# Performance work log

Hardware: AMD Instinct MI355X
Metric: run time of the kernel (lower is better)

The kernel has to match this reference:

```python
import jax, jax.numpy as jnp
import numpy as np

TOPK, ALPHA, BETA, EPS = 13, 1.0, 6.0, 1e-9


def _iou(gt, pr):
    # gt: [B,n,4] xyxy, pr: [B,L,4] xyxy -> [B,n,L]
    gx1, gy1, gx2, gy2 = [gt[..., i][:, :, None] for i in range(4)]
    px1, py1, px2, py2 = [pr[..., i][:, None, :] for i in range(4)]
    iw = jnp.maximum(jnp.minimum(gx2, px2) - jnp.maximum(gx1, px1), 0.0)
    ih = jnp.maximum(jnp.minimum(gy2, py2) - jnp.maximum(gy1, py1), 0.0)
    inter = iw * ih
    area_g = (gx2 - gx1) * (gy2 - gy1)
    area_p = (px2 - px1) * (py2 - py1)
    return inter / (area_g + area_p - inter + 1e-9)


def _points_in_gts(points, gt):
    # points: [L,2], gt: [B,n,4] -> float mask [B,n,L]
    x = points[:, 0][None, None, :]
    y = points[:, 1][None, None, :]
    x1, y1, x2, y2 = [gt[..., i][:, :, None] for i in range(4)]
    dmin = jnp.minimum(jnp.minimum(x - x1, y - y1), jnp.minimum(x2 - x, y2 - y))
    return (dmin > EPS).astype(gt.dtype)


def _gather_topk_anchors(metrics, pad_gt_mask):
    # metrics: [B,n,L] -> float mask [B,n,L] of top-k anchors per gt
    B, n, L = metrics.shape
    _, topk_idxs = jax.lax.top_k(metrics, TOPK)            # [B,n,TOPK]
    mask = pad_gt_mask.astype(bool)                        # [B,n,1]
    topk_idxs = jnp.where(mask, topk_idxs, 0)
    base = (jnp.arange(B * n) * L).reshape(B, n, 1)
    flat = (topk_idxs + base).reshape(-1)
    counts = jnp.zeros(B * n * L, metrics.dtype).at[flat].add(1.0).reshape(B, n, L)
    # anchors hit more than once (only possible via masked-to-0 dup) are dropped
    return jnp.where(counts > 1, 0.0, counts)


def _assigner(pred_scores, pred_bboxes, anchor_points, gt_labels, gt_bboxes, pad_gt_mask, bg_index):
    B, L, C = pred_scores.shape
    n = gt_bboxes.shape[1]
    lbl = gt_labels[..., 0]                                # [B,n]

    ious = _iou(gt_bboxes, pred_bboxes)                    # [B,n,L]
    # bbox_cls_scores[b,g,l] = pred_scores[b,l,gt_labels[b,g]]
    bbox_cls_scores = jnp.take_along_axis(
        pred_scores.transpose(0, 2, 1),                    # [B,C,L]
        jnp.broadcast_to(lbl[:, :, None], (B, n, L)), axis=1)
    align = (bbox_cls_scores ** ALPHA) * (ious ** BETA)    # [B,n,L]

    is_in_gts = _points_in_gts(anchor_points, gt_bboxes)   # [B,n,L]
    is_in_topk = _gather_topk_anchors(align * is_in_gts, pad_gt_mask)
    mask_pos = is_in_topk * is_in_gts * pad_gt_mask        # [B,n,L]
    mask_pos_sum = mask_pos.sum(axis=-2)                   # [B,L]

    # resolve anchors assigned to multiple gts by max IoU (no-op where sum<=1)
    is_max_iou = (jnp.argmax(ious, axis=1)[:, None, :]
                  == jnp.arange(n)[None, :, None]).astype(ious.dtype)
    mask_pos = jnp.where(mask_pos_sum[:, None, :] > 1, is_max_iou, mask_pos)
    mask_pos_sum = mask_pos.sum(axis=-2)

    agi = jnp.argmax(mask_pos, axis=-2)                    # [B,L]
    assigned_labels = jnp.take_along_axis(lbl, agi, axis=1)
    assigned_labels = jnp.where(mask_pos_sum > 0, assigned_labels,
                                jnp.full_like(assigned_labels, bg_index))
    assigned_bboxes = jnp.take_along_axis(
        gt_bboxes, jnp.broadcast_to(agi[..., None], (B, L, 4)), axis=1)

    oh = jax.nn.one_hot(assigned_labels, C + 1, dtype=pred_scores.dtype)
    keep = jnp.array([i for i in range(C + 1) if i != bg_index])
    assigned_scores = oh[..., keep]                        # [B,L,C]

    # rescale alignment metrics per gt instance
    align = align * mask_pos
    max_m = align.max(axis=-1, keepdims=True)              # [B,n,1]
    max_i = (ious * mask_pos).max(axis=-1, keepdims=True)  # [B,n,1]
    align = align / (max_m + EPS) * max_i
    assigned_scores = assigned_scores * align.max(axis=-2)[..., None]
    return assigned_labels, assigned_bboxes, assigned_scores


def setup_inputs() -> dict:
    key = jax.random.key(0)
    ks = jax.random.split(key, 7)
    B, L, C, n = 16, 8400, 80, 128
    pred_scores = jax.random.uniform(ks[0], (B, L, C), jnp.float32)
    anchor_points = jax.random.uniform(ks[1], (L, 2), jnp.float32) * 640.0
    pc = jax.random.uniform(ks[2], (B, L, 2), jnp.float32) * 640.0
    pwh = jax.random.uniform(ks[3], (B, L, 2), jnp.float32) * 64.0 + 4.0
    pred_bboxes = jnp.concatenate([pc - pwh * 0.5, pc + pwh * 0.5], -1)
    gc = jax.random.uniform(ks[4], (B, n, 2), jnp.float32) * 640.0
    gwh = jax.random.uniform(ks[5], (B, n, 2), jnp.float32) * 128.0 + 8.0
    gt_bboxes = jnp.concatenate([gc - gwh * 0.5, gc + gwh * 0.5], -1)
    gt_labels = jax.random.randint(ks[6], (B, n, 1), 0, C)
    pad_gt_mask = jnp.ones((B, n, 1), jnp.float32)
    return {"pred_scores": pred_scores, "pred_bboxes": pred_bboxes,
            "anchor_points": anchor_points, "gt_labels": gt_labels,
            "gt_bboxes": gt_bboxes, "pad_gt_mask": pad_gt_mask, "bg_index": 80}


def reference(pred_scores, pred_bboxes, anchor_points, gt_labels, gt_bboxes, pad_gt_mask, bg_index):
    return _assigner(pred_scores, pred_bboxes, anchor_points, gt_labels,
                     gt_bboxes, pad_gt_mask, bg_index)
```

## Files before the change

kernel.cpp:

```cpp
#include <hip/hip_runtime.h>
#include <cstdint>

#define NTOPK 13
#define FEPS 1e-9f
#define CAP 64
#define GSPLIT 4
#define MASKED_FLAG (1 << 30)

__device__ __forceinline__ float tal_metric(int l, float4 gb, float ag,
                                            const float4* __restrict__ pb,
                                            const float* __restrict__ ps,
                                            const float2* __restrict__ apt,
                                            int C) {
    float2 a = apt[l];
    float dmin = fminf(fminf(a.x - gb.x, a.y - gb.y),
                       fminf(gb.z - a.x, gb.w - a.y));
    float m = 0.0f;
    if (dmin > FEPS) {
        float4 p = pb[l];
        float iw = fmaxf(fminf(gb.z, p.z) - fmaxf(gb.x, p.x), 0.0f);
        float ih = fmaxf(fminf(gb.w, p.w) - fmaxf(gb.y, p.y), 0.0f);
        float inter = iw * ih;
        float ap2 = (p.z - p.x) * (p.w - p.y);
        float iou = inter / (((ag + ap2) - inter) + 1e-9f);
        m = ps[(size_t)l * C] * powf(iou, 6.0f);
    }
    return m;
}

__global__ __launch_bounds__(256) void k_scan(
        const float* __restrict__ pred_scores,
        const float4* __restrict__ pred_bboxes,
        const float2* __restrict__ anchor_points,
        const int* __restrict__ gt_labels,
        const float4* __restrict__ gt_bboxes,
        const float* __restrict__ pad_gt_mask,
        uint64_t* __restrict__ keys,
        uint32_t* __restrict__ cnt,
        uint32_t* __restrict__ maskbits,
        unsigned long long* __restrict__ iou_key,
        int B, int L, int C, int n, int W) {
    int b = blockIdx.y;
    int l0 = blockIdx.x * 256;
    int per = (n + GSPLIT - 1) / GSPLIT;
    int gbeg = blockIdx.z * per;
    int gend = min(n, gbeg + per);
    int ng = gend - gbeg;

    extern __shared__ char smem[];
    float4* sbox = (float4*)smem;
    int*    slab = (int*)(sbox + per);

    for (int i = threadIdx.x; i < ng; i += 256) {
        int g = gbeg + i;
        sbox[i] = gt_bboxes[(size_t)b * n + g];
        int lm = gt_labels[(size_t)b * n + g];
        if (pad_gt_mask[(size_t)b * n + g] == 0.0f) lm |= MASKED_FLAG;
        slab[i] = lm;
    }
    if (blockIdx.z == 0) {
        int rows = min(256, L - l0);
        uint32_t* mb = maskbits + ((size_t)b * L + l0) * W;
        for (int w = threadIdx.x; w < rows * W; w += 256) mb[w] = 0;
    }
    __syncthreads();

    int l = l0 + threadIdx.x;
    if (l >= L) return;
    float2 a = anchor_points[l];
    float4 p = pred_bboxes[(size_t)b * L + l];
    float ap = (p.z - p.x) * (p.w - p.y);
    const float* ps = pred_scores + ((size_t)b * L + l) * C;

    unsigned long long bestkey = 0ull;
    for (int i = 0; i < ng; ++i) {
        float4 gb = sbox[i];
        float iw = fmaxf(fminf(gb.z, p.z) - fmaxf(gb.x, p.x), 0.0f);
        float ih = fmaxf(fminf(gb.w, p.w) - fmaxf(gb.y, p.y), 0.0f);
        float inter = iw * ih;
        float ag = (gb.z - gb.x) * (gb.w - gb.y);
        float iou = inter / (((ag + ap) - inter) + 1e-9f);
        int g = gbeg + i;
        unsigned long long akey =
            ((unsigned long long)__float_as_uint(iou) << 32) | (uint32_t)(~g);
        if (akey > bestkey) bestkey = akey;

        int lm = slab[i];
        if (!(lm & MASKED_FLAG) && inter > 0.0f) {
            float dmin = fminf(fminf(a.x - gb.x, a.y - gb.y),
                               fminf(gb.z - a.x, gb.w - a.y));
            if (dmin > FEPS) {
                float m = ps[lm] * powf(iou, 6.0f);
                if (m > 0.0f) {
                    int bg = b * n + g;
                    uint32_t off = atomicAdd(&cnt[bg], 1u);
                    if (off < CAP)
                        keys[(size_t)bg * CAP + off] =
                            ((uint64_t)__float_as_uint(m) << 32) | (uint32_t)(~l);
                }
            }
        }
    }
    atomicMax(&iou_key[(size_t)b * L + l], bestkey);
}

__global__ __launch_bounds__(256) void k_select(
        const float* __restrict__ pred_scores,
        const float4* __restrict__ pred_bboxes,
        const float2* __restrict__ anchor_points,
        const int* __restrict__ gt_labels,
        const float4* __restrict__ gt_bboxes,
        const float* __restrict__ pad_gt_mask,
        const uint64_t* __restrict__ keys,
        const uint32_t* __restrict__ cnt,
        uint32_t* __restrict__ maskbits,
        int B, int L, int C, int n, int W) {
    int wid = threadIdx.x >> 6;
    int lane = threadIdx.x & 63;
    int bg = blockIdx.x * 4 + wid;
    if (bg >= B * n) return;
    if (pad_gt_mask[bg] == 0.0f) return;
    int b = bg / n;
    int g = bg - b * n;

    uint32_t p = cnt[bg];
    int mypick = -1;

    if (p <= CAP) {
        uint64_t mykey = (lane < (int)p) ? keys[(size_t)bg * CAP + lane] : 0ull;
        int np = min((int)p, NTOPK);
        for (int k = 0; k < np; ++k) {
            uint64_t mk = mykey;
            for (int s = 1; s < 64; s <<= 1) {
                uint64_t o = __shfl_xor((unsigned long long)mk, s);
                if (o > mk) mk = o;
            }
            if (lane == k) mypick = (int)~(uint32_t)mk;
            if (mykey == mk) mykey = 0ull;
        }
        int fill = np, c = 0;
        while (fill < NTOPK) {
            bool inP = __ballot(lane < np && mypick == c) != 0ull;
            if (!inP) {
                if (lane == fill) mypick = c;
                ++fill;
            }
            ++c;
        }
    } else {
        float4 gb = gt_bboxes[bg];
        float ag = (gb.z - gb.x) * (gb.w - gb.y);
        const float4* pb = pred_bboxes + (size_t)b * L;
        const float*  ps = pred_scores + ((size_t)b * L) * C + gt_labels[bg];
        for (int k = 0; k < NTOPK; ++k) {
            uint64_t bk = 0;
            for (int l = lane; l < L; l += 64) {
                bool taken = false;
                for (int j = 0; j < k; ++j)
                    taken |= (__shfl(mypick, j) == l);
                if (taken) continue;
                float m = tal_metric(l, gb, ag, pb, ps, anchor_points, C);
                uint64_t key = ((uint64_t)__float_as_uint(m) << 32) | (uint32_t)(~l);
                if (key > bk) bk = key;
            }
            for (int s = 1; s < 64; s <<= 1) {
                uint64_t o = __shfl_xor((unsigned long long)bk, s);
                if (o > bk) bk = o;
            }
            if (lane == k) mypick = (int)~(uint32_t)bk;
        }
    }

    if (lane < NTOPK) {
        int l = mypick;
        float4 gb = gt_bboxes[bg];
        float2 a = anchor_points[l];
        float dmin = fminf(fminf(a.x - gb.x, a.y - gb.y),
                           fminf(gb.z - a.x, gb.w - a.y));
        if (dmin > FEPS) {
            atomicOr(&maskbits[((size_t)b * L + l) * W + (g >> 5)],
                     1u << (g & 31));
        }
    }
}

__global__ __launch_bounds__(256) void k_assign(
        const float* __restrict__ pred_scores,
        const float4* __restrict__ pred_bboxes,
        const float4* __restrict__ gt_bboxes,
        const int* __restrict__ gt_labels,
        const uint32_t* __restrict__ maskbits,
        const unsigned long long* __restrict__ iou_key,
        const int* __restrict__ bg_ptr,
        int* __restrict__ assigned_g,
        float* __restrict__ align_val,
        uint32_t* __restrict__ max_m,
        uint32_t* __restrict__ max_i,
        float* __restrict__ out_labels,
        float4* __restrict__ out_bboxes,
        int B, int L, int C, int n, int W) {
    int idx = blockIdx.x * blockDim.x + threadIdx.x;
    if (idx >= B * L) return;
    int b = idx / L;

    int sum = 0, firstg = -1;
    for (int w = 0; w < W; ++w) {
        uint32_t bits = maskbits[(size_t)idx * W + w];
        if (bits && firstg < 0) firstg = w * 32 + __ffs(bits) - 1;
        sum += __popc(bits);
    }

    int g;
    if (sum == 0) g = -1;
    else if (sum == 1) g = firstg;
    else g = (int)~(uint32_t)iou_key[idx];
    assigned_g[idx] = g;

    float av = 0.0f;
    if (g >= 0) {
        float4 p = pred_bboxes[idx];
        float ap = (p.z - p.x) * (p.w - p.y);
        float4 gb = gt_bboxes[(size_t)b * n + g];
        float iw = fmaxf(fminf(gb.z, p.z) - fmaxf(gb.x, p.x), 0.0f);
        float ih = fmaxf(fminf(gb.w, p.w) - fmaxf(gb.y, p.y), 0.0f);
        float inter = iw * ih;
        float ag = (gb.z - gb.x) * (gb.w - gb.y);
        float iou = inter / (((ag + ap) - inter) + 1e-9f);
        int label = gt_labels[(size_t)b * n + g];
        float score = pred_scores[(size_t)idx * C + label];
        av = score * powf(iou, 6.0f);
        atomicMax(&max_m[(size_t)b * n + g], __float_as_uint(av));
        atomicMax(&max_i[(size_t)b * n + g], __float_as_uint(iou));
        out_labels[idx] = (float)label;
        out_bboxes[idx] = gb;
    } else {
        out_labels[idx] = (float)(*bg_ptr);
        out_bboxes[idx] = gt_bboxes[(size_t)b * n];
    }
    align_val[idx] = av;
}

__global__ __launch_bounds__(256) void k_scores4(
        const int* __restrict__ assigned_g,
        const float* __restrict__ align_val,
        const uint32_t* __restrict__ max_m,
        const uint32_t* __restrict__ max_i,
        const int* __restrict__ gt_labels,
        const int* __restrict__ bg_ptr,
        float4* __restrict__ out_scores,
        int B, int L, int C, int n, int total4) {
    int idx = blockIdx.x * blockDim.x + threadIdx.x;
    if (idx >= total4) return;
    int C4 = C >> 2;
    int c0 = (idx % C4) * 4;
    int bl = idx / C4;
    int g = assigned_g[bl];
    float4 v = make_float4(0.f, 0.f, 0.f, 0.f);
    if (g >= 0) {
        int b = bl / L;
        int label = gt_labels[(size_t)b * n + g];
        int bgi = *bg_ptr;
        float mm = __uint_as_float(max_m[(size_t)b * n + g]);
        float mi = __uint_as_float(max_i[(size_t)b * n + g]);
        float val = align_val[bl] / (mm + FEPS) * mi;
        int cls0 = (c0     < bgi) ? c0     : c0 + 1;
        int cls1 = (c0 + 1 < bgi) ? c0 + 1 : c0 + 2;
        int cls2 = (c0 + 2 < bgi) ? c0 + 2 : c0 + 3;
        int cls3 = (c0 + 3 < bgi) ? c0 + 3 : c0 + 4;
        if (cls0 == label) v.x = val;
        if (cls1 == label) v.y = val;
        if (cls2 == label) v.z = val;
        if (cls3 == label) v.w = val;
    }
    out_scores[idx] = v;
}

__global__ __launch_bounds__(256) void k_scores1(
        const int* __restrict__ assigned_g,
        const float* __restrict__ align_val,
        const uint32_t* __restrict__ max_m,
        const uint32_t* __restrict__ max_i,
        const int* __restrict__ gt_labels,
        const int* __restrict__ bg_ptr,
        float* __restrict__ out_scores,
        int B, int L, int C, int n, int total) {
    int idx = blockIdx.x * blockDim.x + threadIdx.x;
    if (idx >= total) return;
    int c = idx % C;
    int bl = idx / C;
    int g = assigned_g[bl];
    float v = 0.0f;
    if (g >= 0) {
        int b = bl / L;
        int label = gt_labels[(size_t)b * n + g];
        int bgi = *bg_ptr;
        int cls = (c < bgi) ? c : c + 1;
        if (cls == label) {
            float mm = __uint_as_float(max_m[(size_t)b * n + g]);
            float mi = __uint_as_float(max_i[(size_t)b * n + g]);
            v = align_val[bl] / (mm + FEPS) * mi;
        }
    }
    out_scores[idx] = v;
}

extern "C" void kernel_launch(void* const* d_in, const int* in_sizes, int n_in,
                              void* d_out, int out_size, void* d_ws, size_t ws_size,
                              hipStream_t stream) {
    const float*  pred_scores   = (const float*)d_in[0];
    const float4* pred_bboxes   = (const float4*)d_in[1];
    const float2* anchor_points = (const float2*)d_in[2];
    const int*    gt_labels     = (const int*)d_in[3];
    const float4* gt_bboxes     = (const float4*)d_in[4];
    const float*  pad_gt_mask   = (const float*)d_in[5];
    const int*    bg_ptr        = (const int*)d_in[6];

    const int L = in_sizes[2] / 2;
    const int B = in_sizes[1] / (L * 4);
    const int C = in_sizes[0] / (B * L);
    const int n = in_sizes[3] / B;
    const int W = (n + 31) / 32;

    char* ws = (char*)d_ws;
    unsigned long long* iou_key = (unsigned long long*)ws;
    ws += (size_t)B * L * sizeof(unsigned long long);
    uint32_t* cnt      = (uint32_t*)ws;  ws += (size_t)B * n * sizeof(uint32_t);
    uint32_t* max_m    = (uint32_t*)ws;  ws += (size_t)B * n * sizeof(uint32_t);
    uint32_t* max_i    = (uint32_t*)ws;  ws += (size_t)B * n * sizeof(uint32_t);
    size_t zbytes = (size_t)((char*)ws - (char*)d_ws);
    uint64_t* keys     = (uint64_t*)ws;  ws += (size_t)B * n * CAP * sizeof(uint64_t);
    uint32_t* maskbits = (uint32_t*)ws;  ws += (size_t)B * L * W * sizeof(uint32_t);
    int*      assigned_g = (int*)ws;     ws += (size_t)B * L * sizeof(int);
    float*    align_val  = (float*)ws;   ws += (size_t)B * L * sizeof(float);

    float*  out_labels = (float*)d_out;
    float4* out_bboxes = (float4*)((float*)d_out + (size_t)B * L);
    float*  out_scores = (float*)d_out + (size_t)B * L * 5;

    hipMemsetAsync(d_ws, 0, zbytes, stream);

    {
        int per = (n + GSPLIT - 1) / GSPLIT;
        dim3 grid((L + 255) / 256, B, GSPLIT);
        size_t smem = (size_t)per * (sizeof(float4) + sizeof(int));
        k_scan<<<grid, 256, smem, stream>>>(
            pred_scores, pred_bboxes, anchor_points, gt_labels, gt_bboxes,
            pad_gt_mask, keys, cnt, maskbits, iou_key, B, L, C, n, W);
    }
    k_select<<<(B * n + 3) / 4, 256, 0, stream>>>(
        pred_scores, pred_bboxes, anchor_points, gt_labels, gt_bboxes,
        pad_gt_mask, keys, cnt, maskbits, B, L, C, n, W);
    k_assign<<<(B * L + 255) / 256, 256, 0, stream>>>(
        pred_scores, pred_bboxes, gt_bboxes, gt_labels, maskbits, iou_key,
        bg_ptr, assigned_g, align_val, max_m, max_i, out_labels, out_bboxes,
        B, L, C, n, W);
    if ((C & 3) == 0) {
        int total4 = B * L * (C >> 2);
        k_scores4<<<(total4 + 255) / 256, 256, 0, stream>>>(
            assigned_g, align_val, max_m, max_i, gt_labels, bg_ptr,
            (float4*)out_scores, B, L, C, n, total4);
    } else {
        int total = B * L * C;
        k_scores1<<<(total + 255) / 256, 256, 0, stream>>>(
            assigned_g, align_val, max_m, max_i, gt_labels, bg_ptr,
            out_scores, B, L, C, n, total);
    }
}
```

Measured before the change: 55.17 us.

## Replace global candidate atomics with per-tile shared-memory slots and packed assignment counters

The scan kernel now processes all GTs per block and collects candidates into per-(gt, tile) fixed slots using shared-memory counters, writing a sentinel when a tile overflows. This removes global atomicAdd contention and the memset. The select kernel merges up to NT*SLOTS keys per lane in registers, falling back to the dense rescan when any tile overflowed. Per-anchor bitmasks are replaced by a packed count+gt atomic counter, and the per-anchor best-IoU is written directly instead of via atomicMax. The cost is fewer blocks in the scan and a dense fallback path that may trigger often when GTs are large.

```diff
diff --git a/kernel.cpp b/kernel.cpp
--- a/kernel.cpp
+++ b/kernel.cpp
@@ -3,9 +3,10 @@
 
 #define NTOPK 13
 #define FEPS 1e-9f
-#define CAP 64
-#define GSPLIT 4
+#define SLOTS 4
+#define KMAX 8
 #define MASKED_FLAG (1 << 30)
+#define SENTINEL 0xFFFFFFFFFFFFFFFFull
 
 __device__ __forceinline__ float tal_metric(int l, float4 gb, float ag,
                                             const float4* __restrict__ pb,
@@ -35,73 +36,86 @@
         const int* __restrict__ gt_labels,
         const float4* __restrict__ gt_bboxes,
         const float* __restrict__ pad_gt_mask,
-        uint64_t* __restrict__ keys,
-        uint32_t* __restrict__ cnt,
-        uint32_t* __restrict__ maskbits,
-        unsigned long long* __restrict__ iou_key,
-        int B, int L, int C, int n, int W) {
+        unsigned long long* __restrict__ keys,
+        unsigned long long* __restrict__ cc,
+        unsigned long long* __restrict__ iou_part,
+        uint32_t* __restrict__ max_m,
+        uint32_t* __restrict__ max_i,
+        int B, int L, int C, int n, int NT) {
     int b = blockIdx.y;
-    int l0 = blockIdx.x * 256;
-    int per = (n + GSPLIT - 1) / GSPLIT;
-    int gbeg = blockIdx.z * per;
-    int gend = min(n, gbeg + per);
-    int ng = gend - gbeg;
+    int tile = blockIdx.x;
+    int l0 = tile * 256;
+    int t = threadIdx.x;
 
     extern __shared__ char smem[];
     float4* sbox = (float4*)smem;
-    int*    slab = (int*)(sbox + per);
-
-    for (int i = threadIdx.x; i < ng; i += 256) {
-        int g = gbeg + i;
-        sbox[i] = gt_bboxes[(size_t)b * n + g];
-        int lm = gt_labels[(size_t)b * n + g];
-        if (pad_gt_mask[(size_t)b * n + g] == 0.0f) lm |= MASKED_FLAG;
+    int*    slab = (int*)(sbox + n);
+    int*    scnt = slab + n;
+
+    for (int i = t; i < n; i += 256) {
+        sbox[i] = gt_bboxes[(size_t)b * n + i];
+        int lm = gt_labels[(size_t)b * n + i];
+        if (pad_gt_mask[(size_t)b * n + i] == 0.0f) lm |= MASKED_FLAG;
         slab[i] = lm;
-    }
-    if (blockIdx.z == 0) {
+        scnt[i] = 0;
+    }
+    {
         int rows = min(256, L - l0);
-        uint32_t* mb = maskbits + ((size_t)b * L + l0) * W;
-        for (int w = threadIdx.x; w < rows * W; w += 256) mb[w] = 0;
+        for (int r = t; r < rows; r += 256) cc[(size_t)b * L + l0 + r] = 0ull;
+        if (tile == 0)
+            for (int i = t; i < 2 * n; i += 256)
+                (i < n ? max_m : max_i)[(size_t)b * n + (i < n ? i : i - n)] = 0u;
     }
     __syncthreads();
 
-    int l = l0 + threadIdx.x;
-    if (l >= L) return;
-    float2 a = anchor_points[l];
-    float4 p = pred_bboxes[(size_t)b * L + l];
-    float ap = (p.z - p.x) * (p.w - p.y);
-    const float* ps = pred_scores + ((size_t)b * L + l) * C;
-
-    unsigned long long bestkey = 0ull;
-    for (int i = 0; i < ng; ++i) {
-        float4 gb = sbox[i];
-        float iw = fmaxf(fminf(gb.z, p.z) - fmaxf(gb.x, p.x), 0.0f);
-        float ih = fmaxf(fminf(gb.w, p.w) - fmaxf(gb.y, p.y), 0.0f);
-        float inter = iw * ih;
-        float ag = (gb.z - gb.x) * (gb.w - gb.y);
-        float iou = inter / (((ag + ap) - inter) + 1e-9f);
-        int g = gbeg + i;
-        unsigned long long akey =
-            ((unsigned long long)__float_as_uint(iou) << 32) | (uint32_t)(~g);
-        if (akey > bestkey) bestkey = akey;
-
-        int lm = slab[i];
-        if (!(lm & MASKED_FLAG) && inter > 0.0f) {
-            float dmin = fminf(fminf(a.x - gb.x, a.y - gb.y),
-                               fminf(gb.z - a.x, gb.w - a.y));
-            if (dmin > FEPS) {
-                float m = ps[lm] * powf(iou, 6.0f);
-                if (m > 0.0f) {
-                    int bg = b * n + g;
-                    uint32_t off = atomicAdd(&cnt[bg], 1u);
-                    if (off < CAP)
-                        keys[(size_t)bg * CAP + off] =
-                            ((uint64_t)__float_as_uint(m) << 32) | (uint32_t)(~l);
+    int l = l0 + t;
+    if (l < L) {
+        float2 a = anchor_points[l];
+        float4 p = pred_bboxes[(size_t)b * L + l];
+        float ap = (p.z - p.x) * (p.w - p.y);
+        const float* ps = pred_scores + ((size_t)b * L + l) * C;
+
+        unsigned long long bestkey = 0ull;
+        for (int i = 0; i < n; ++i) {
+            float4 gb = sbox[i];
+            float iw = fmaxf(fminf(gb.z, p.z) - fmaxf(gb.x, p.x), 0.0f);
+            float ih = fmaxf(fminf(gb.w, p.w) - fmaxf(gb.y, p.y), 0.0f);
+            float inter = iw * ih;
+            unsigned long long akey = (unsigned long long)(uint32_t)(~i);
+            int lm = slab[i];
+            if (inter > 0.0f) {
+                float ag = (gb.z - gb.x) * (gb.w - gb.y);
+                float iou = inter / (((ag + ap) - inter) + 1e-9f);
+                akey |= (unsigned long long)__float_as_uint(iou) << 32;
+                if (!(lm & MASKED_FLAG)) {
+                    float dmin = fminf(fminf(a.x - gb.x, a.y - gb.y),
+                                       fminf(gb.z - a.x, gb.w - a.y));
+                    if (dmin > FEPS) {
+                        float m = ps[lm] * powf(iou, 6.0f);
+                        if (m > 0.0f) {
+                            int slot = atomicAdd(&scnt[i], 1);
+                            if (slot < SLOTS)
+                                keys[(((size_t)(b * n + i)) * NT + tile) * SLOTS + slot] =
+                                    ((unsigned long long)__float_as_uint(m) << 32) |
+                                    (uint32_t)(~l);
+                        }
+                    }
                 }
             }
-        }
-    }
-    atomicMax(&iou_key[(size_t)b * L + l], bestkey);
+            if (akey > bestkey) bestkey = akey;
+        }
+        iou_part[(size_t)b * L + l] = bestkey;
+    }
+    __syncthreads();
+
+    for (int s = t; s < n * SLOTS; s += 256) {
+        int g = s / SLOTS, j = s - g * SLOTS;
+        int c = scnt[g];
+        unsigned long long* dst =
+            &keys[(((size_t)(b * n + g)) * NT + tile) * SLOTS + j];
+        if (c > SLOTS && j == 0) *dst = SENTINEL;
+        else if (j >= c) *dst = 0ull;
+    }
 }
 
 __global__ __launch_bounds__(256) void k_select(
@@ -111,10 +125,9 @@
         const int* __restrict__ gt_labels,
         const float4* __restrict__ gt_bboxes,
         const float* __restrict__ pad_gt_mask,
-        const uint64_t* __restrict__ keys,
-        const uint32_t* __restrict__ cnt,
-        uint32_t* __restrict__ maskbits,
-        int B, int L, int C, int n, int W) {
+        const unsigned long long* __restrict__ keys,
+        unsigned long long* __restrict__ cc,
+        int B, int L, int C, int n, int NT) {
     int wid = threadIdx.x >> 6;
     int lane = threadIdx.x & 63;
     int bg = blockIdx.x * 4 + wid;
@@ -123,63 +136,84 @@
     int b = bg / n;
     int g = bg - b * n;
 
-    uint32_t p = cnt[bg];
+    int TK = NT * SLOTS;
     int mypick = -1;
-
-    if (p <= CAP) {
-        uint64_t mykey = (lane < (int)p) ? keys[(size_t)bg * CAP + lane] : 0ull;
-        int np = min((int)p, NTOPK);
-        for (int k = 0; k < np; ++k) {
-            uint64_t mk = mykey;
-            for (int s = 1; s < 64; s <<= 1) {
-                uint64_t o = __shfl_xor((unsigned long long)mk, s);
-                if (o > mk) mk = o;
-            }
-            if (lane == k) mypick = (int)~(uint32_t)mk;
-            if (mykey == mk) mykey = 0ull;
-        }
-        int fill = np, c = 0;
-        while (fill < NTOPK) {
-            bool inP = __ballot(lane < np && mypick == c) != 0ull;
-            if (!inP) {
-                if (lane == fill) mypick = c;
-                ++fill;
-            }
-            ++c;
-        }
-    } else {
+    bool dense = (TK > 64 * KMAX);
+
+    if (!dense) {
+        unsigned long long lk[KMAX];
+        int nk = 0;
+        bool sent = false;
+        for (int s = lane; s < TK; s += 64) {
+            unsigned long long k = keys[(size_t)bg * TK + s];
+            if (k == SENTINEL) sent = true;
+            lk[nk++] = k;
+        }
+        for (int j = nk; j < KMAX; ++j) lk[j] = 0ull;
+        dense = (__ballot(sent) != 0ull);
+
+        if (!dense) {
+            int np = 0;
+            for (int k = 0; k < NTOPK; ++k) {
+                unsigned long long mk = 0ull;
+                #pragma unroll
+                for (int j = 0; j < KMAX; ++j) mk = (lk[j] > mk) ? lk[j] : mk;
+                for (int s = 1; s < 64; s <<= 1) {
+                    unsigned long long o = __shfl_xor(mk, s);
+                    if (o > mk) mk = o;
+                }
+                if (mk == 0ull) break;
+                #pragma unroll
+                for (int j = 0; j < KMAX; ++j) if (lk[j] == mk) lk[j] = 0ull;
+                if (lane == k) mypick = (int)~(uint32_t)mk;
+                ++np;
+            }
+            int fill = np, c = 0;
+            while (fill < NTOPK) {
+                bool inP = __ballot(lane < np && mypick == c) != 0ull;
+                if (!inP) {
+                    if (lane == fill) mypick = c;
+                    ++fill;
+                }
+                ++c;
+            }
+        }
+    }
+
+    if (dense) {
         float4 gb = gt_bboxes[bg];
         float ag = (gb.z - gb.x) * (gb.w - gb.y);
         const float4* pb = pred_bboxes + (size_t)b * L;
         const float*  ps = pred_scores + ((size_t)b * L) * C + gt_labels[bg];
         for (int k = 0; k < NTOPK; ++k) {
-            uint64_t bk = 0;
+            unsigned long long bk = 0ull;
             for (int l = lane; l < L; l += 64) {
                 bool taken = false;
                 for (int j = 0; j < k; ++j)
                     taken |= (__shfl(mypick, j) == l);
                 if (taken) continue;
                 float m = tal_metric(l, gb, ag, pb, ps, anchor_points, C);
-                uint64_t key = ((uint64_t)__float_as_uint(m) << 32) | (uint32_t)(~l);
+                unsigned long long key =
+                    ((unsigned long long)__float_as_uint(m) << 32) | (uint32_t)(~l);
                 if (key > bk) bk = key;
             }
             for (int s = 1; s < 64; s <<= 1) {
-                uint64_t o = __shfl_xor((unsigned long long)bk, s);
+                unsigned long long o = __shfl_xor(bk, s);
                 if (o > bk) bk = o;
             }
             if (lane == k) mypick = (int)~(uint32_t)bk;
         }
     }
 
-    if (lane < NTOPK) {
+    if (lane < NTOPK && mypick >= 0) {
         int l = mypick;
         float4 gb = gt_bboxes[bg];
         float2 a = anchor_points[l];
         float dmin = fminf(fminf(a.x - gb.x, a.y - gb.y),
                            fminf(gb.z - a.x, gb.w - a.y));
         if (dmin > FEPS) {
-            atomicOr(&maskbits[((size_t)b * L + l) * W + (g >> 5)],
-                     1u << (g & 31));
+            atomicAdd(&cc[(size_t)b * L + l],
+                      (1ull << 32) | (unsigned long long)(uint32_t)(g + 1));
         }
     }
 }
@@ -189,8 +223,8 @@
         const float4* __restrict__ pred_bboxes,
         const float4* __restrict__ gt_bboxes,
         const int* __restrict__ gt_labels,
-        const uint32_t* __restrict__ maskbits,
-        const unsigned long long* __restrict__ iou_key,
+        const unsigned long long* __restrict__ cc,
+        const unsigned long long* __restrict__ iou_part,
         const int* __restrict__ bg_ptr,
         int* __restrict__ assigned_g,
         float* __restrict__ align_val,
@@ -198,22 +232,17 @@
         uint32_t* __restrict__ max_i,
         float* __restrict__ out_labels,
         float4* __restrict__ out_bboxes,
-        int B, int L, int C, int n, int W) {
+        int B, int L, int C, int n) {
     int idx = blockIdx.x * blockDim.x + threadIdx.x;
     if (idx >= B * L) return;
     int b = idx / L;
 
-    int sum = 0, firstg = -1;
-    for (int w = 0; w < W; ++w) {
-        uint32_t bits = maskbits[(size_t)idx * W + w];
-        if (bits && firstg < 0) firstg = w * 32 + __ffs(bits) - 1;
-        sum += __popc(bits);
-    }
-
+    unsigned long long w = cc[idx];
+    int count = (int)(w >> 32);
     int g;
-    if (sum == 0) g = -1;
-    else if (sum == 1) g = firstg;
-    else g = (int)~(uint32_t)iou_key[idx];
+    if (count == 0) g = -1;
+    else if (count == 1) g = (int)(uint32_t)w - 1;
+    else g = (int)~(uint32_t)iou_part[idx];
     assigned_g[idx] = g;
 
     float av = 0.0f;
@@ -319,17 +348,17 @@
     const int B = in_sizes[1] / (L * 4);
     const int C = in_sizes[0] / (B * L);
     const int n = in_sizes[3] / B;
-    const int W = (n + 31) / 32;
+    const int NT = (L + 255) / 256;
 
     char* ws = (char*)d_ws;
-    unsigned long long* iou_key = (unsigned long long*)ws;
+    unsigned long long* keys = (unsigned long long*)ws;
+    ws += (size_t)B * n * NT * SLOTS * sizeof(unsigned long long);
+    unsigned long long* cc = (unsigned long long*)ws;
     ws += (size_t)B * L * sizeof(unsigned long long);
-    uint32_t* cnt      = (uint32_t*)ws;  ws += (size_t)B * n * sizeof(uint32_t);
+    unsigned long long* iou_part = (unsigned long long*)ws;
+    ws += (size_t)B * L * sizeof(unsigned long long);
     uint32_t* max_m    = (uint32_t*)ws;  ws += (size_t)B * n * sizeof(uint32_t);
     uint32_t* max_i    = (uint32_t*)ws;  ws += (size_t)B * n * sizeof(uint32_t);
-    size_t zbytes = (size_t)((char*)ws - (char*)d_ws);
-    uint64_t* keys     = (uint64_t*)ws;  ws += (size_t)B * n * CAP * sizeof(uint64_t);
-    uint32_t* maskbits = (uint32_t*)ws;  ws += (size_t)B * L * W * sizeof(uint32_t);
     int*      assigned_g = (int*)ws;     ws += (size_t)B * L * sizeof(int);
     float*    align_val  = (float*)ws;   ws += (size_t)B * L * sizeof(float);
 
@@ -337,23 +366,20 @@
     float4* out_bboxes = (float4*)((float*)d_out + (size_t)B * L);
     float*  out_scores = (float*)d_out + (size_t)B * L * 5;
 
-    hipMemsetAsync(d_ws, 0, zbytes, stream);
-
     {
-        int per = (n + GSPLIT - 1) / GSPLIT;
-        dim3 grid((L + 255) / 256, B, GSPLIT);
-        size_t smem = (size_t)per * (sizeof(float4) + sizeof(int));
+        dim3 grid(NT, B);
+        size_t smem = (size_t)n * (sizeof(float4) + 2 * sizeof(int));
         k_scan<<<grid, 256, smem, stream>>>(
             pred_scores, pred_bboxes, anchor_points, gt_labels, gt_bboxes,
-            pad_gt_mask, keys, cnt, maskbits, iou_key, B, L, C, n, W);
+            pad_gt_mask, keys, cc, iou_part, max_m, max_i, B, L, C, n, NT);
     }
     k_select<<<(B * n + 3) / 4, 256, 0, stream>>>(
         pred_scores, pred_bboxes, anchor_points, gt_labels, gt_bboxes,
-        pad_gt_mask, keys, cnt, maskbits, B, L, C, n, W);
+        pad_gt_mask, keys, cc, B, L, C, n, NT);
     k_assign<<<(B * L + 255) / 256, 256, 0, stream>>>(
-        pred_scores, pred_bboxes, gt_bboxes, gt_labels, maskbits, iou_key,
+        pred_scores, pred_bboxes, gt_bboxes, gt_labels, cc, iou_part,
         bg_ptr, assigned_g, align_val, max_m, max_i, out_labels, out_bboxes,
-        B, L, C, n, W);
+        B, L, C, n);
     if ((C & 3) == 0) {
         int total4 = B * L * (C >> 2);
         k_scores4<<<(total4 + 255) / 256, 256, 0, stream>>>(
```

After: 65.55 us. 18.8% more time.
